# Performance work log

Measured on AMD Instinct MI355X. Metric: run time of the kernel, lower is better.

Reference implementation:

```python
import jax, jax.numpy as jnp
import numpy as np

MAX_VALUE = 127.0  # signed 8-bit: 2**(8-1)-1


def _quantize_int8(t, amax):
    # per-tensor symmetric quantization: round(x * 127/amax), clamped to [-127, 127]
    scale = MAX_VALUE / amax
    return jnp.clip(jnp.round(t * scale), -MAX_VALUE, MAX_VALUE).astype(jnp.int8)


def setup_inputs() -> dict:
    key = jax.random.key(0)
    k1, k2, k3 = jax.random.split(key, 3)
    N, K, M = 8192, 4096, 4096
    x = jax.random.normal(k1, (N, K), dtype=jnp.float32)
    weight = jax.random.normal(k2, (M, K), dtype=jnp.float32) * (1.0 / np.sqrt(K))
    bias = jax.random.normal(k3, (M,), dtype=jnp.float32) * (1.0 / np.sqrt(K))
    return {"x": x, "weight": weight, "bias": bias}


def reference(x, weight, bias):
    # amax from max-abs calibration (per-tensor), as TensorQuantizer would hold
    amax = jnp.max(jnp.abs(x))
    amax_w = jnp.max(jnp.abs(weight))
    qi = _quantize_int8(x, amax)          # [N, K] int8
    qw = _quantize_int8(weight, amax_w)   # [M, K] int8
    acc = jnp.matmul(qi.astype(jnp.int32), qw.astype(jnp.int32).T)  # [N, M] int32
    # dequant: output / ((max/amax) * (max/amax_w)), then bias
    dequant = (amax * amax_w) / (MAX_VALUE * MAX_VALUE)
    return acc.astype(jnp.float32) * dequant + bias
```

## Files before the change

### kernel.cpp

```cpp
#include <hip/hip_runtime.h>

#define K_DIM 4096
#define N_DIM 8192
#define M_DIM 4096

typedef int v4i __attribute__((ext_vector_type(4)));

__global__ void amax_kernel(const float4* __restrict__ p, int n4,
                            unsigned* __restrict__ out) {
  int tid = blockIdx.x * blockDim.x + threadIdx.x;
  int stride = gridDim.x * blockDim.x;
  float m = 0.f;
  for (int i = tid; i < n4; i += stride) {
    float4 v = p[i];
    m = fmaxf(m, fmaxf(fmaxf(fabsf(v.x), fabsf(v.y)),
                       fmaxf(fabsf(v.z), fabsf(v.w))));
  }
#pragma unroll
  for (int off = 32; off > 0; off >>= 1)
    m = fmaxf(m, __shfl_down(m, off));
  __shared__ float sm[4];
  int lane = threadIdx.x & 63, w = threadIdx.x >> 6;
  if (lane == 0) sm[w] = m;
  __syncthreads();
  if (threadIdx.x == 0) {
    m = fmaxf(fmaxf(sm[0], sm[1]), fmaxf(sm[2], sm[3]));
    atomicMax(out, __float_as_uint(m));
  }
}

__global__ void quant_kernel(const float4* __restrict__ in, int* __restrict__ out,
                             int n4, const unsigned* __restrict__ amax_bits) {
  float scale = 127.0f / __uint_as_float(*amax_bits);
  int tid = blockIdx.x * blockDim.x + threadIdx.x;
  int stride = gridDim.x * blockDim.x;
  for (int i = tid; i < n4; i += stride) {
    float4 v = in[i];
    int q0 = (int)fminf(fmaxf(rintf(v.x * scale), -127.f), 127.f);
    int q1 = (int)fminf(fmaxf(rintf(v.y * scale), -127.f), 127.f);
    int q2 = (int)fminf(fmaxf(rintf(v.z * scale), -127.f), 127.f);
    int q3 = (int)fminf(fmaxf(rintf(v.w * scale), -127.f), 127.f);
    unsigned packed = (unsigned)(q0 & 255) | ((unsigned)(q1 & 255) << 8) |
                      ((unsigned)(q2 & 255) << 16) | ((unsigned)(q3 & 255) << 24);
    out[i] = (int)packed;
  }
}

__device__ __forceinline__ void gld_lds16(const void* g, void* l) {
  __builtin_amdgcn_global_load_lds(
      (const __attribute__((address_space(1))) void*)g,
      (__attribute__((address_space(3))) void*)l, 16, 0, 0);
}

__global__ __launch_bounds__(256, 2) void gemm_i8(
    const signed char* __restrict__ A,
    const signed char* __restrict__ B,
    const float* __restrict__ bias,
    float* __restrict__ out,
    const unsigned* __restrict__ scal)
{
  __shared__ signed char la[128 * 64];
  __shared__ signed char lb[128 * 64];

  const int tid = threadIdx.x;
  const int lane = tid & 63;
  const int w = tid >> 6;
  const int wr = (w & 1) * 64;
  const int wc = (w >> 1) * 64;
  const long r0 = (long)blockIdx.x * 128;
  const long c0 = (long)blockIdx.y * 128;

  const int srow = tid >> 2;
  const int scol = (tid & 3) * 16;
  const signed char* ga0 = A + (r0 + srow) * K_DIM + scol;
  const signed char* ga1 = A + (r0 + 64 + srow) * K_DIM + scol;
  const signed char* gb0 = B + (c0 + srow) * K_DIM + scol;
  const signed char* gb1 = B + (c0 + 64 + srow) * K_DIM + scol;
  signed char* la0 = la + tid * 16;
  signed char* la1 = la + 4096 + tid * 16;
  signed char* lb0 = lb + tid * 16;
  signed char* lb1 = lb + 4096 + tid * 16;

  v4i acc[4][4];
#pragma unroll
  for (int i = 0; i < 4; ++i)
#pragma unroll
    for (int j = 0; j < 4; ++j) acc[i][j] = (v4i){0, 0, 0, 0};

  const int fr = lane & 15;
  const int fq = lane >> 4;

  for (int k0 = 0; k0 < K_DIM; k0 += 64) {
    gld_lds16(ga0 + k0, la0);
    gld_lds16(ga1 + k0, la1);
    gld_lds16(gb0 + k0, lb0);
    gld_lds16(gb1 + k0, lb1);
    __syncthreads();

    v4i av[4], bv[4];
#pragma unroll
    for (int i = 0; i < 4; ++i)
      av[i] = *(const v4i*)(la + (wr + i * 16 + fr) * 64 + fq * 16);
#pragma unroll
    for (int j = 0; j < 4; ++j)
      bv[j] = *(const v4i*)(lb + (wc + j * 16 + fr) * 64 + fq * 16);
#pragma unroll
    for (int i = 0; i < 4; ++i)
#pragma unroll
      for (int j = 0; j < 4; ++j)
        acc[i][j] = __builtin_amdgcn_mfma_i32_16x16x64_i8(av[i], bv[j],
                                                          acc[i][j], 0, 0, 0);
    __syncthreads();
  }

  const float dq =
      (__uint_as_float(scal[0]) * __uint_as_float(scal[1])) / 16129.0f;
  float bs[4];
#pragma unroll
  for (int j = 0; j < 4; ++j) bs[j] = bias[c0 + wc + j * 16 + fr];

#pragma unroll
  for (int i = 0; i < 4; ++i) {
    const long rbase = r0 + wr + i * 16 + fq * 4;
#pragma unroll
    for (int j = 0; j < 4; ++j) {
      const long c = c0 + wc + j * 16 + fr;
#pragma unroll
      for (int t = 0; t < 4; ++t) {
        out[(rbase + t) * (long)M_DIM + c] = (float)acc[i][j][t] * dq + bs[j];
      }
    }
  }
}

extern "C" void kernel_launch(void* const* d_in, const int* in_sizes, int n_in,
                              void* d_out, int out_size, void* d_ws, size_t ws_size,
                              hipStream_t stream) {
  const float* x = (const float*)d_in[0];
  const float* wt = (const float*)d_in[1];
  const float* bias = (const float*)d_in[2];
  float* out = (float*)d_out;

  unsigned* scal = (unsigned*)d_ws;
  signed char* qx = (signed char*)d_ws + 256;
  signed char* qw = qx + (long)N_DIM * K_DIM;

  hipMemsetAsync(d_ws, 0, 16, stream);

  const int n4x = N_DIM * K_DIM / 4;
  const int n4w = M_DIM * K_DIM / 4;
  amax_kernel<<<2048, 256, 0, stream>>>((const float4*)x, n4x, scal + 0);
  amax_kernel<<<1024, 256, 0, stream>>>((const float4*)wt, n4w, scal + 1);
  quant_kernel<<<2048, 256, 0, stream>>>((const float4*)x, (int*)qx, n4x, scal + 0);
  quant_kernel<<<1024, 256, 0, stream>>>((const float4*)wt, (int*)qw, n4w, scal + 1);

  dim3 grid(N_DIM / 128, M_DIM / 128);
  gemm_i8<<<grid, 256, 0, stream>>>(qx, qw, bias, out, scal);
}
```

Before: 483.0 us.

## Merge prepass kernels, widen quant stores, double GEMM K-tile with XOR LDS swizzle

The amax and quantization passes for x and weight are each merged into a single launch, which cuts the launch count from four to two. The quant kernel now writes 16 bytes per thread instead of 4. The GEMM K-tile grows from 64 to 128, halving the number of barrier pairs per output tile. LDS chunks are XOR-swizzled by row to reduce bank conflicts on the fragment reads. LDS use doubles to 32KB per block, which may affect occupancy at 2 blocks per CU.

```diff
diff --git a/kernel.cpp b/kernel.cpp
--- a/kernel.cpp
+++ b/kernel.cpp
@@ -6,10 +6,20 @@
 
 typedef int v4i __attribute__((ext_vector_type(4)));
 
-__global__ void amax_kernel(const float4* __restrict__ p, int n4,
-                            unsigned* __restrict__ out) {
-  int tid = blockIdx.x * blockDim.x + threadIdx.x;
-  int stride = gridDim.x * blockDim.x;
+__global__ void amax2_kernel(const float4* __restrict__ x,
+                             const float4* __restrict__ w,
+                             unsigned* __restrict__ scal) {
+  const int XB = 2048, WB = 1024;
+  const float4* p;
+  int n4, b, nb;
+  unsigned* out;
+  if (blockIdx.x < XB) {
+    p = x; n4 = N_DIM * K_DIM / 4; out = scal + 0; b = blockIdx.x; nb = XB;
+  } else {
+    p = w; n4 = M_DIM * K_DIM / 4; out = scal + 1; b = blockIdx.x - XB; nb = WB;
+  }
+  int tid = b * blockDim.x + threadIdx.x;
+  int stride = nb * blockDim.x;
   float m = 0.f;
   for (int i = tid; i < n4; i += stride) {
     float4 v = p[i];
@@ -20,8 +30,8 @@
   for (int off = 32; off > 0; off >>= 1)
     m = fmaxf(m, __shfl_down(m, off));
   __shared__ float sm[4];
-  int lane = threadIdx.x & 63, w = threadIdx.x >> 6;
-  if (lane == 0) sm[w] = m;
+  int lane = threadIdx.x & 63, wv = threadIdx.x >> 6;
+  if (lane == 0) sm[wv] = m;
   __syncthreads();
   if (threadIdx.x == 0) {
     m = fmaxf(fmaxf(sm[0], sm[1]), fmaxf(sm[2], sm[3]));
@@ -29,20 +39,45 @@
   }
 }
 
-__global__ void quant_kernel(const float4* __restrict__ in, int* __restrict__ out,
-                             int n4, const unsigned* __restrict__ amax_bits) {
-  float scale = 127.0f / __uint_as_float(*amax_bits);
-  int tid = blockIdx.x * blockDim.x + threadIdx.x;
-  int stride = gridDim.x * blockDim.x;
-  for (int i = tid; i < n4; i += stride) {
-    float4 v = in[i];
-    int q0 = (int)fminf(fmaxf(rintf(v.x * scale), -127.f), 127.f);
-    int q1 = (int)fminf(fmaxf(rintf(v.y * scale), -127.f), 127.f);
-    int q2 = (int)fminf(fmaxf(rintf(v.z * scale), -127.f), 127.f);
-    int q3 = (int)fminf(fmaxf(rintf(v.w * scale), -127.f), 127.f);
-    unsigned packed = (unsigned)(q0 & 255) | ((unsigned)(q1 & 255) << 8) |
-                      ((unsigned)(q2 & 255) << 16) | ((unsigned)(q3 & 255) << 24);
-    out[i] = (int)packed;
+__device__ __forceinline__ unsigned pack4(float4 v, float s) {
+  int q0 = (int)fminf(fmaxf(rintf(v.x * s), -127.f), 127.f);
+  int q1 = (int)fminf(fmaxf(rintf(v.y * s), -127.f), 127.f);
+  int q2 = (int)fminf(fmaxf(rintf(v.z * s), -127.f), 127.f);
+  int q3 = (int)fminf(fmaxf(rintf(v.w * s), -127.f), 127.f);
+  return (unsigned)(q0 & 255) | ((unsigned)(q1 & 255) << 8) |
+         ((unsigned)(q2 & 255) << 16) | ((unsigned)(q3 & 255) << 24);
+}
+
+__global__ void quant2_kernel(const float4* __restrict__ x,
+                              const float4* __restrict__ w,
+                              int4* __restrict__ qx, int4* __restrict__ qw,
+                              const unsigned* __restrict__ scal) {
+  const int XB = 2048, WB = 1024;
+  const float4* in;
+  int4* out;
+  int n16, b, nb;
+  float amax;
+  if (blockIdx.x < XB) {
+    in = x; out = qx; n16 = N_DIM * K_DIM / 16; b = blockIdx.x; nb = XB;
+    amax = __uint_as_float(scal[0]);
+  } else {
+    in = w; out = qw; n16 = M_DIM * K_DIM / 16; b = blockIdx.x - XB; nb = WB;
+    amax = __uint_as_float(scal[1]);
+  }
+  float s = 127.0f / amax;
+  int tid = b * blockDim.x + threadIdx.x;
+  int stride = nb * blockDim.x;
+  for (int i = tid; i < n16; i += stride) {
+    float4 v0 = in[4 * i + 0];
+    float4 v1 = in[4 * i + 1];
+    float4 v2 = in[4 * i + 2];
+    float4 v3 = in[4 * i + 3];
+    int4 o;
+    o.x = (int)pack4(v0, s);
+    o.y = (int)pack4(v1, s);
+    o.z = (int)pack4(v2, s);
+    o.w = (int)pack4(v3, s);
+    out[i] = o;
   }
 }
 
@@ -59,8 +94,8 @@
     float* __restrict__ out,
     const unsigned* __restrict__ scal)
 {
-  __shared__ signed char la[128 * 64];
-  __shared__ signed char lb[128 * 64];
+  __shared__ signed char la[128 * 128];
+  __shared__ signed char lb[128 * 128];
 
   const int tid = threadIdx.x;
   const int lane = tid & 63;
@@ -70,16 +105,10 @@
   const long r0 = (long)blockIdx.x * 128;
   const long c0 = (long)blockIdx.y * 128;
 
-  const int srow = tid >> 2;
-  const int scol = (tid & 3) * 16;
-  const signed char* ga0 = A + (r0 + srow) * K_DIM + scol;
-  const signed char* ga1 = A + (r0 + 64 + srow) * K_DIM + scol;
-  const signed char* gb0 = B + (c0 + srow) * K_DIM + scol;
-  const signed char* gb1 = B + (c0 + 64 + srow) * K_DIM + scol;
-  signed char* la0 = la + tid * 16;
-  signed char* la1 = la + 4096 + tid * 16;
-  signed char* lb0 = lb + tid * 16;
-  signed char* lb1 = lb + 4096 + tid * 16;
+  const int srow = tid >> 3;
+  const int gcol = ((tid & 7) ^ (srow & 7)) * 16;
+  const signed char* ga = A + (r0 + srow) * K_DIM + gcol;
+  const signed char* gb = B + (c0 + srow) * K_DIM + gcol;
 
   v4i acc[4][4];
 #pragma unroll
@@ -89,27 +118,34 @@
 
   const int fr = lane & 15;
   const int fq = lane >> 4;
+  const int sa = fr & 7;
 
-  for (int k0 = 0; k0 < K_DIM; k0 += 64) {
-    gld_lds16(ga0 + k0, la0);
-    gld_lds16(ga1 + k0, la1);
-    gld_lds16(gb0 + k0, lb0);
-    gld_lds16(gb1 + k0, lb1);
+  for (int k0 = 0; k0 < K_DIM; k0 += 128) {
+#pragma unroll
+    for (int p = 0; p < 4; ++p) {
+      gld_lds16(ga + (long)p * 32 * K_DIM + k0, la + p * 4096 + tid * 16);
+      gld_lds16(gb + (long)p * 32 * K_DIM + k0, lb + p * 4096 + tid * 16);
+    }
     __syncthreads();
 
-    v4i av[4], bv[4];
 #pragma unroll
-    for (int i = 0; i < 4; ++i)
-      av[i] = *(const v4i*)(la + (wr + i * 16 + fr) * 64 + fq * 16);
+    for (int ks = 0; ks < 2; ++ks) {
+      v4i av[4], bv[4];
 #pragma unroll
-    for (int j = 0; j < 4; ++j)
-      bv[j] = *(const v4i*)(lb + (wc + j * 16 + fr) * 64 + fq * 16);
-#pragma unroll
-    for (int i = 0; i < 4; ++i)
+      for (int i = 0; i < 4; ++i)
+        av[i] = *(const v4i*)(la + (wr + i * 16 + fr) * 128 +
+                              (((ks * 4 + fq) ^ sa) * 16));
 #pragma unroll
       for (int j = 0; j < 4; ++j)
-        acc[i][j] = __builtin_amdgcn_mfma_i32_16x16x64_i8(av[i], bv[j],
-                                                          acc[i][j], 0, 0, 0);
+        bv[j] = *(const v4i*)(lb + (wc + j * 16 + fr) * 128 +
+                              (((ks * 4 + fq) ^ sa) * 16));
+#pragma unroll
+      for (int i = 0; i < 4; ++i)
+#pragma unroll
+        for (int j = 0; j < 4; ++j)
+          acc[i][j] = __builtin_amdgcn_mfma_i32_16x16x64_i8(av[i], bv[j],
+                                                            acc[i][j], 0, 0, 0);
+    }
     __syncthreads();
   }
 
@@ -147,12 +183,10 @@
 
   hipMemsetAsync(d_ws, 0, 16, stream);
 
-  const int n4x = N_DIM * K_DIM / 4;
-  const int n4w = M_DIM * K_DIM / 4;
-  amax_kernel<<<2048, 256, 0, stream>>>((const float4*)x, n4x, scal + 0);
-  amax_kernel<<<1024, 256, 0, stream>>>((const float4*)wt, n4w, scal + 1);
-  quant_kernel<<<2048, 256, 0, stream>>>((const float4*)x, (int*)qx, n4x, scal + 0);
-  quant_kernel<<<1024, 256, 0, stream>>>((const float4*)wt, (int*)qw, n4w, scal + 1);
+  amax2_kernel<<<3072, 256, 0, stream>>>((const float4*)x, (const float4*)wt,
+                                         scal);
+  quant2_kernel<<<3072, 256, 0, stream>>>((const float4*)x, (const float4*)wt,
+                                          (int4*)qx, (int4*)qw, scal);
 
   dim3 grid(N_DIM / 128, M_DIM / 128);
   gemm_i8<<<grid, 256, 0, stream>>>(qx, qw, bias, out, scal);
```

Measured after the change: 441.1 us. -8.7%, faster.
